# Kernel tuning notes

Hardware: AMD Instinct MI355X
Metric: run time of the kernel (lower is better)

Reference implementation:

```python
import jax, jax.numpy as jnp
import numpy as np

NUM_MODELS = 64
OUT_F = 256
IN_F = 256
B = 32768
F0 = 2
F1 = 2


def setup_inputs() -> dict:
    key = jax.random.key(0)
    k1, k2, k3, k4 = jax.random.split(key, 4)
    sqrt_k = float(np.sqrt(1.0 / NUM_MODELS))
    weights = 2 * sqrt_k * jax.random.uniform(k1, (NUM_MODELS, OUT_F, IN_F), dtype=jnp.float32) - sqrt_k
    biases = 2 * sqrt_k * jax.random.uniform(k2, (NUM_MODELS, OUT_F), dtype=jnp.float32) - sqrt_k
    inputs = jax.random.normal(k3, (B, IN_F // F1), dtype=jnp.float32)
    indices = jax.random.randint(k4, (B,), 0, NUM_MODELS, dtype=jnp.int64)
    return {"inputs": inputs, "weights": weights, "biases": biases,
            "indices": indices, "factor0": F0, "factor1": F1}


def reference(inputs, weights, biases, indices, factor0, factor1):
    out_sub = weights.shape[1] // factor0
    in_sub = weights.shape[2] // factor1
    # Gather per-sample weight slices: (B, out_sub, in_sub)
    subweight = weights[indices, :out_sub, :in_sub]
    subbias = biases[indices, :out_sub]  # (B, out_sub)
    # Batched matvec + bias
    return jnp.einsum('boi,bi->bo', subweight, inputs) + subbias
```

## Files before the change

### kernel.cpp

```cpp
#include <hip/hip_runtime.h>
#include <hip/hip_bf16.h>

#define NMODELS 64
#define NB      32768
#define INF     256
#define OUTF    256
#define INS     128
#define OUTS    128
#define TILE_M  64
#define NT      10
#define NSB     128
#define WCONV_BLOCKS 512
#define POISON  0xAAAAAAAAu

typedef unsigned int u32;
typedef unsigned short u16;
using bf16x8  = __attribute__((ext_vector_type(8))) short;
using f32x4   = __attribute__((ext_vector_type(4))) float;
using float4v = __attribute__((ext_vector_type(4))) float;
using short8v = __attribute__((ext_vector_type(8))) short;

__device__ __forceinline__ u16 f2bf(float f) {
    union { float fv; u32 u; } v; v.fv = f;
    u32 u = v.u;
    u += 0x7fffu + ((u >> 16) & 1u);
    return (u16)(u >> 16);
}

__device__ __forceinline__ void async_copy16(const void* g, void* l) {
    __builtin_amdgcn_global_load_lds((const __attribute__((address_space(1))) u32*)g,
                                     (__attribute__((address_space(3))) u32*)l,
                                     16, 0, 0);
}

__global__ __launch_bounds__(256) void k_scatconv(const int* __restrict__ idx,
                                                  const float* __restrict__ w,
                                                  u32* __restrict__ cursors,
                                                  int* __restrict__ perm,
                                                  u16* __restrict__ wb) {
    const int t = threadIdx.x;
    const int b = blockIdx.x;
    if (b < NSB) {
        __shared__ int h[NMODELS];
        __shared__ int base[NMODELS];
        if (t < NMODELS) h[t] = 0;
        __syncthreads();
        const int i = b * 256 + t;
        const int m = idx[i];
        const int r = atomicAdd(&h[m], 1);
        __syncthreads();
        if (t < NMODELS && h[t] != 0)
            base[t] = (int)(atomicAdd(&cursors[t], (u32)h[t]) - POISON);
        __syncthreads();
        perm[(m << 10) + base[m] + r] = i;
    } else {
        const int cid = (b - NSB) * 256 + t;
        const int m   = cid >> 11;
        const int rem = cid & 2047;
        const int row = rem >> 4;
        const int c   = rem & 15;
        const float* src = w + ((size_t)m * OUTF + row) * INF + c * 8;
        float4v v0 = *(const float4v*)(src);
        float4v v1 = *(const float4v*)(src + 4);
        short8v s;
        s[0]=(short)f2bf(v0.x); s[1]=(short)f2bf(v0.y); s[2]=(short)f2bf(v0.z); s[3]=(short)f2bf(v0.w);
        s[4]=(short)f2bf(v1.x); s[5]=(short)f2bf(v1.y); s[6]=(short)f2bf(v1.z); s[7]=(short)f2bf(v1.w);
        *(short8v*)(wb + ((size_t)(m * 128 + row) * 128) + ((c ^ (row & 15)) * 8)) = s;
    }
}

__global__ __launch_bounds__(256) void k_gemm(const float* __restrict__ x,
                                              const u16* __restrict__ wb,
                                              const float* __restrict__ bias,
                                              const u32* __restrict__ cursors,
                                              const int* __restrict__ perm,
                                              float* __restrict__ out) {
    __shared__ __align__(16) u16 Ws[OUTS * 128];
    const int m   = blockIdx.x;
    const int cnt = (int)(cursors[m] - POISON);
    if ((int)blockIdx.y * TILE_M >= cnt) return;
    const int t    = threadIdx.x;
    const int wave = t >> 6;
    const int lane = t & 63;
    const int quad = lane >> 4;
    const int lr   = lane & 15;

    {
        const char* g = (const char*)(wb + (size_t)m * (OUTS * 128));
        char* l = (char*)Ws;
        #pragma unroll
        for (int itc = 0; itc < 8; ++itc) {
            const int off = itc * 4096 + wave * 1024;
            async_copy16(g + off + lane * 16, l + off);
        }
    }
    float4v bv4[8];
    #pragma unroll
    for (int nt = 0; nt < 8; ++nt)
        bv4[nt] = *(const float4v*)(bias + m * OUTF + nt * 16 + quad * 4);

    int xoff[4];
    #pragma unroll
    for (int k0 = 0; k0 < 4; ++k0) xoff[k0] = ((k0 * 4 + quad) ^ lr) * 8;
    const int rowbase = lr * 128;
    const int pbase   = m << 10;

    int tile = blockIdx.y;
    int row  = tile * TILE_M + wave * 16 + lr;
    int p    = (row < cnt) ? perm[pbase + row] : -1;
    const float* xr = x + (size_t)((p < 0) ? 0 : p) * INS + quad * 8;
    float4v xa[8];
    #pragma unroll
    for (int k0 = 0; k0 < 4; ++k0) {
        xa[2 * k0]     = *(const float4v*)(xr + k0 * 32);
        xa[2 * k0 + 1] = *(const float4v*)(xr + k0 * 32 + 4);
    }

    __syncthreads();

    for (;;) {
        bf16x8 xb[4];
        #pragma unroll
        for (int k0 = 0; k0 < 4; ++k0) {
            bf16x8 a;
            a[0] = (short)f2bf(xa[2*k0].x);   a[1] = (short)f2bf(xa[2*k0].y);
            a[2] = (short)f2bf(xa[2*k0].z);   a[3] = (short)f2bf(xa[2*k0].w);
            a[4] = (short)f2bf(xa[2*k0+1].x); a[5] = (short)f2bf(xa[2*k0+1].y);
            a[6] = (short)f2bf(xa[2*k0+1].z); a[7] = (short)f2bf(xa[2*k0+1].w);
            xb[k0] = a;
        }
        f32x4 acc[8];
        #pragma unroll
        for (int nt = 0; nt < 8; ++nt) acc[nt] = (f32x4){0.f, 0.f, 0.f, 0.f};
        #pragma unroll
        for (int k0 = 0; k0 < 4; ++k0) {
            #pragma unroll
            for (int nt = 0; nt < 8; ++nt) {
                bf16x8 wfr = *(const bf16x8*)&Ws[nt * 2048 + rowbase + xoff[k0]];
                acc[nt] = __builtin_amdgcn_mfma_f32_16x16x32_bf16(wfr, xb[k0], acc[nt], 0, 0, 0);
            }
        }
        const int curp = p;
        const int ntile = tile + NT;
        const bool more = (ntile * TILE_M < cnt);
        if (more) {
            row = ntile * TILE_M + wave * 16 + lr;
            p   = (row < cnt) ? perm[pbase + row] : -1;
            const float* xr2 = x + (size_t)((p < 0) ? 0 : p) * INS + quad * 8;
            #pragma unroll
            for (int k0 = 0; k0 < 4; ++k0) {
                xa[2 * k0]     = *(const float4v*)(xr2 + k0 * 32);
                xa[2 * k0 + 1] = *(const float4v*)(xr2 + k0 * 32 + 4);
            }
        }
        if (curp >= 0) {
            float* orow = out + (size_t)curp * OUTS + quad * 4;
            #pragma unroll
            for (int nt = 0; nt < 8; ++nt)
                *(float4v*)(orow + nt * 16) = acc[nt] + bv4[nt];
        }
        if (!more) break;
        tile = ntile;
    }
}

extern "C" void kernel_launch(void* const* d_in, const int* in_sizes, int n_in,
                              void* d_out, int out_size, void* d_ws, size_t ws_size,
                              hipStream_t stream) {
    const float* x    = (const float*)d_in[0];
    const float* w    = (const float*)d_in[1];
    const float* bias = (const float*)d_in[2];
    const int*   idx  = (const int*)d_in[3];
    float* out = (float*)d_out;

    int* ws      = (int*)d_ws;
    u32* cursors = (u32*)ws;
    int* perm    = ws + 64;
    u16* wb      = (u16*)(ws + 64 + 65536);

    k_scatconv<<<dim3(NSB + WCONV_BLOCKS), dim3(256), 0, stream>>>(idx, w, cursors, perm, wb);
    k_gemm    <<<dim3(NMODELS, NT),        dim3(256), 0, stream>>>(x, wb, bias, cursors, perm, out);
}
```

Baseline: 93.56 us.

## Pre-convert inputs to bf16 and scatter into model-sorted order before GEMM

Result: slower. 98.11 us (+4.9%).

```diff
diff --git a/kernel.cpp b/kernel.cpp
--- a/kernel.cpp
+++ b/kernel.cpp
@@ -18,6 +18,7 @@
 using bf16x8  = __attribute__((ext_vector_type(8))) short;
 using f32x4   = __attribute__((ext_vector_type(4))) float;
 using float4v = __attribute__((ext_vector_type(4))) float;
+using short4v = __attribute__((ext_vector_type(4))) short;
 using short8v = __attribute__((ext_vector_type(8))) short;
 
 __device__ __forceinline__ u16 f2bf(float f) {
@@ -34,15 +35,18 @@
 }
 
 __global__ __launch_bounds__(256) void k_scatconv(const int* __restrict__ idx,
+                                                  const float* __restrict__ x,
                                                   const float* __restrict__ w,
                                                   u32* __restrict__ cursors,
                                                   int* __restrict__ perm,
-                                                  u16* __restrict__ wb) {
+                                                  u16* __restrict__ wb,
+                                                  u16* __restrict__ xp) {
     const int t = threadIdx.x;
     const int b = blockIdx.x;
     if (b < NSB) {
         __shared__ int h[NMODELS];
         __shared__ int base[NMODELS];
+        __shared__ int slotL[256];
         if (t < NMODELS) h[t] = 0;
         __syncthreads();
         const int i = b * 256 + t;
@@ -52,7 +56,20 @@
         if (t < NMODELS && h[t] != 0)
             base[t] = (int)(atomicAdd(&cursors[t], (u32)h[t]) - POISON);
         __syncthreads();
-        perm[(m << 10) + base[m] + r] = i;
+        const int slot = (m << 10) + base[m] + r;
+        perm[slot] = i;
+        slotL[t]   = slot;
+        __syncthreads();
+        const int l32 = t & 31;
+        const int sg  = t >> 5;
+        for (int it = 0; it < 32; ++it) {
+            const int s = it * 8 + sg;
+            float4v v = *(const float4v*)(x + (size_t)(b * 256 + s) * INS + l32 * 4);
+            short4v o;
+            o.x = (short)f2bf(v.x); o.y = (short)f2bf(v.y);
+            o.z = (short)f2bf(v.z); o.w = (short)f2bf(v.w);
+            *(short4v*)(xp + (size_t)slotL[s] * INS + l32 * 4) = o;
+        }
     } else {
         const int cid = (b - NSB) * 256 + t;
         const int m   = cid >> 11;
@@ -69,7 +86,7 @@
     }
 }
 
-__global__ __launch_bounds__(256) void k_gemm(const float* __restrict__ x,
+__global__ __launch_bounds__(256) void k_gemm(const u16* __restrict__ xp,
                                               const u16* __restrict__ wb,
                                               const float* __restrict__ bias,
                                               const u32* __restrict__ cursors,
@@ -106,29 +123,16 @@
     const int pbase   = m << 10;
 
     int tile = blockIdx.y;
-    int row  = tile * TILE_M + wave * 16 + lr;
-    int p    = (row < cnt) ? perm[pbase + row] : -1;
-    const float* xr = x + (size_t)((p < 0) ? 0 : p) * INS + quad * 8;
-    float4v xa[8];
+    int srow = pbase + tile * TILE_M + wave * 16 + lr;
+    int p    = perm[srow];
+    const u16* xr = xp + (size_t)srow * INS + quad * 8;
+    bf16x8 xb[4];
     #pragma unroll
-    for (int k0 = 0; k0 < 4; ++k0) {
-        xa[2 * k0]     = *(const float4v*)(xr + k0 * 32);
-        xa[2 * k0 + 1] = *(const float4v*)(xr + k0 * 32 + 4);
-    }
+    for (int k0 = 0; k0 < 4; ++k0) xb[k0] = *(const bf16x8*)(xr + k0 * 32);
 
     __syncthreads();
 
     for (;;) {
-        bf16x8 xb[4];
-        #pragma unroll
-        for (int k0 = 0; k0 < 4; ++k0) {
-            bf16x8 a;
-            a[0] = (short)f2bf(xa[2*k0].x);   a[1] = (short)f2bf(xa[2*k0].y);
-            a[2] = (short)f2bf(xa[2*k0].z);   a[3] = (short)f2bf(xa[2*k0].w);
-            a[4] = (short)f2bf(xa[2*k0+1].x); a[5] = (short)f2bf(xa[2*k0+1].y);
-            a[6] = (short)f2bf(xa[2*k0+1].z); a[7] = (short)f2bf(xa[2*k0+1].w);
-            xb[k0] = a;
-        }
         f32x4 acc[8];
         #pragma unroll
         for (int nt = 0; nt < 8; ++nt) acc[nt] = (f32x4){0.f, 0.f, 0.f, 0.f};
@@ -144,14 +148,11 @@
         const int ntile = tile + NT;
         const bool more = (ntile * TILE_M < cnt);
         if (more) {
-            row = ntile * TILE_M + wave * 16 + lr;
-            p   = (row < cnt) ? perm[pbase + row] : -1;
-            const float* xr2 = x + (size_t)((p < 0) ? 0 : p) * INS + quad * 8;
+            srow = pbase + ntile * TILE_M + wave * 16 + lr;
+            p    = perm[srow];
+            const u16* xr2 = xp + (size_t)srow * INS + quad * 8;
             #pragma unroll
-            for (int k0 = 0; k0 < 4; ++k0) {
-                xa[2 * k0]     = *(const float4v*)(xr2 + k0 * 32);
-                xa[2 * k0 + 1] = *(const float4v*)(xr2 + k0 * 32 + 4);
-            }
+            for (int k0 = 0; k0 < 4; ++k0) xb[k0] = *(const bf16x8*)(xr2 + k0 * 32);
         }
         if (curp >= 0) {
             float* orow = out + (size_t)curp * OUTS + quad * 4;
@@ -177,7 +178,8 @@
     u32* cursors = (u32*)ws;
     int* perm    = ws + 64;
     u16* wb      = (u16*)(ws + 64 + 65536);
+    u16* xp      = wb + (size_t)NMODELS * OUTS * 128;
 
-    k_scatconv<<<dim3(NSB + WCONV_BLOCKS), dim3(256), 0, stream>>>(idx, w, cursors, perm, wb);
-    k_gemm    <<<dim3(NMODELS, NT),        dim3(256), 0, stream>>>(x, wb, bias, cursors, perm, out);
+    k_scatconv<<<dim3(NSB + WCONV_BLOCKS), dim3(256), 0, stream>>>(idx, x, w, cursors, perm, wb, xp);
+    k_gemm    <<<dim3(NMODELS, NT),        dim3(256), 0, stream>>>(xp, wb, bias, cursors, perm, out);
 }
```
